# Performance work log

Measured on AMD Instinct MI355X. Metric: run time of the kernel, lower is better.

## Reference

```python
import jax, jax.numpy as jnp
import numpy as np

NUM_CLASSES = 10


def setup_inputs() -> dict:
    key = jax.random.key(0)
    k1, k2, k3 = jax.random.split(key, 3)
    N, M, D = 1024, 50000, 512
    x = jax.random.normal(k1, (N, D), dtype=jnp.float32)
    exemplars = jax.random.normal(k2, (M, D), dtype=jnp.float32)
    labels = jax.random.randint(k3, (M,), 0, NUM_CLASSES)
    Sigma_inv = jnp.ones((D,), dtype=jnp.float32)
    beta = jnp.ones((1,), dtype=jnp.float32)
    gamma = jnp.ones((1,), dtype=jnp.float32)
    return {"x": x, "exemplars": exemplars, "labels": labels,
            "Sigma_inv": Sigma_inv, "beta": beta, "gamma": gamma}


def reference(x, exemplars, labels, Sigma_inv, beta, gamma):
    # Weighted squared Mahalanobis distance via expanded quadratic form:
    # dist[n,m] = sum_d Sigma_inv[d] * (x[n,d] - e[m,d])^2
    #           = (x^2 @ S) + (e^2 @ S) - 2 * (x*S) @ e^T
    x_sq = jnp.einsum('nd,d->n', x * x, Sigma_inv)            # [N]
    e_sq = jnp.einsum('md,d->m', exemplars * exemplars, Sigma_inv)  # [M]
    cross = jnp.einsum('nd,md->nm', x * Sigma_inv, exemplars)  # [N, M]
    distances = x_sq[:, None] + e_sq[None, :] - 2.0 * cross    # [N, M]
    attention = jnp.exp(-beta[0] * distances)                  # [N, M]
    # Per-class masked sum == segment sum over exemplar labels.
    logits = jax.ops.segment_sum(attention.T, labels,
                                 num_segments=NUM_CLASSES).T   # [N, 10]
    return jax.nn.softmax(gamma[0] * logits, axis=1)
```

## Files before the change

### kernel.cpp

```cpp
#include <hip/hip_runtime.h>
#include <hip/hip_bf16.h>
#include <stdint.h>
#include <stddef.h>

#define N_TOT 1024
#define M_TOT 50000
#define M_PAD 50048
#define D_TOT 512
#define NC    10

typedef __attribute__((ext_vector_type(8))) __bf16 bf16x8;
typedef __attribute__((ext_vector_type(4))) float f32x4;
typedef __attribute__((ext_vector_type(4))) unsigned int u32x4;

union Frag16 { u32x4 q; bf16x8 b; unsigned short u[8]; };
union Pack8  { u32x4 q; unsigned short u[8]; };

__device__ __forceinline__ unsigned short f2bf(float x) {
  unsigned int u = __float_as_uint(x);
  unsigned int r = (u + 0x7fffu + ((u >> 16) & 1u)) >> 16;
  return (unsigned short)r;
}

__device__ __forceinline__ void gld_lds16(const void* g, void* l) {
  auto gp = (__attribute__((address_space(1))) unsigned int*)(uintptr_t)g;
  auto lp = (__attribute__((address_space(3))) unsigned int*)(uintptr_t)l;
  __builtin_amdgcn_global_load_lds(gp, lp, 16, 0, 0);
}

__global__ void prep_rows(const float* __restrict__ e, const float* __restrict__ x,
                          const float* __restrict__ S,
                          unsigned short* __restrict__ eb, unsigned short* __restrict__ xb,
                          float* __restrict__ e_sq, float* __restrict__ x_sq) {
  const int lane = threadIdx.x & 63;
  const int wid  = threadIdx.x >> 6;
  const int row  = blockIdx.x * 4 + wid;
  const int d0   = lane * 8;

  float4 s0 = *(const float4*)(S + d0);
  float4 s1 = *(const float4*)(S + d0 + 4);
  float ss[8] = {s0.x, s0.y, s0.z, s0.w, s1.x, s1.y, s1.z, s1.w};

  float acc = 0.f;
  Pack8 o;

  if (row < M_PAD) {
    if (row < M_TOT) {
      const float* src = e + (size_t)row * D_TOT + d0;
      float4 v0 = *(const float4*)src;
      float4 v1 = *(const float4*)(src + 4);
      float vv[8] = {v0.x, v0.y, v0.z, v0.w, v1.x, v1.y, v1.z, v1.w};
      #pragma unroll
      for (int j = 0; j < 8; ++j) { acc += ss[j] * vv[j] * vv[j]; o.u[j] = f2bf(vv[j]); }
    } else {
      #pragma unroll
      for (int j = 0; j < 8; ++j) o.u[j] = 0;
      acc = 0.f;
    }
    *(u32x4*)(eb + (size_t)row * D_TOT + d0) = o.q;
    #pragma unroll
    for (int off = 32; off; off >>= 1) acc += __shfl_down(acc, off);
    if (lane == 0) e_sq[row] = (row < M_TOT) ? acc : 1e30f;
  } else {
    const int xr = row - M_PAD;
    const float* src = x + (size_t)xr * D_TOT + d0;
    float4 v0 = *(const float4*)src;
    float4 v1 = *(const float4*)(src + 4);
    float vv[8] = {v0.x, v0.y, v0.z, v0.w, v1.x, v1.y, v1.z, v1.w};
    #pragma unroll
    for (int j = 0; j < 8; ++j) {
      float w = ss[j] * vv[j];
      acc += w * vv[j];
      o.u[j] = f2bf(w);
    }
    *(u32x4*)(xb + (size_t)xr * D_TOT + d0) = o.q;
    #pragma unroll
    for (int off = 32; off; off >>= 1) acc += __shfl_down(acc, off);
    if (lane == 0) x_sq[xr] = acc;
  }
}

__global__ void zero_f32(float* __restrict__ p, int n) {
  int i = blockIdx.x * 256 + threadIdx.x;
  if (i < n) p[i] = 0.f;
}

__launch_bounds__(256)
__global__ void gemm_fused(const unsigned short* __restrict__ xb,
                           const unsigned short* __restrict__ eb,
                           const float* __restrict__ x_sq, const float* __restrict__ e_sq,
                           const int* __restrict__ labels,
                           const float* __restrict__ betap,
                           float* __restrict__ logits) {
  __shared__ unsigned short As[2][128 * 32];
  __shared__ unsigned short Bs[2][128 * 32];
  __shared__ float cls[128 * NC];

  const int tid  = threadIdx.x;
  const int lane = tid & 63;
  const int wid  = tid >> 6;
  const int wr   = wid >> 1, wc = wid & 1;
  const int nt   = blockIdx.x;
  const int mt   = blockIdx.y;

  const int cA0 = wid * 128 + lane;
  const int cA1 = cA0 + 64;
  const unsigned short* gA0 = xb + (size_t)(nt * 128 + (cA0 >> 2)) * D_TOT + (cA0 & 3) * 8;
  const unsigned short* gA1 = xb + (size_t)(nt * 128 + (cA1 >> 2)) * D_TOT + (cA1 & 3) * 8;
  const unsigned short* gB0 = eb + (size_t)(mt * 128 + (cA0 >> 2)) * D_TOT + (cA0 & 3) * 8;
  const unsigned short* gB1 = eb + (size_t)(mt * 128 + (cA1 >> 2)) * D_TOT + (cA1 & 3) * 8;

  const f32x4 vzero = {0.f, 0.f, 0.f, 0.f};
  f32x4 acc[4][4];
  #pragma unroll
  for (int i = 0; i < 4; ++i)
    #pragma unroll
    for (int j = 0; j < 4; ++j) acc[i][j] = vzero;

  const int arow = wr * 64 + (lane & 15);
  const int brow = wc * 64 + (lane & 15);
  const int koff = (lane >> 4) * 8;

  #define STAGE(BUF, K0)                                    \
    do {                                                    \
      gld_lds16(gA0 + (K0), &As[(BUF)][cA0 * 8]);           \
      gld_lds16(gA1 + (K0), &As[(BUF)][cA1 * 8]);           \
      gld_lds16(gB0 + (K0), &Bs[(BUF)][cA0 * 8]);           \
      gld_lds16(gB1 + (K0), &Bs[(BUF)][cA1 * 8]);           \
    } while (0)

  #define COMPUTE(BUF)                                                            \
    do {                                                                          \
      Frag16 fa[4], fb[4];                                                        \
      _Pragma("unroll")                                                           \
      for (int i = 0; i < 4; ++i)                                                 \
        fa[i].q = *(const u32x4*)(&As[(BUF)][(arow + i * 16) * 32 + koff]);       \
      _Pragma("unroll")                                                           \
      for (int j = 0; j < 4; ++j)                                                 \
        fb[j].q = *(const u32x4*)(&Bs[(BUF)][(brow + j * 16) * 32 + koff]);       \
      _Pragma("unroll")                                                           \
      for (int i = 0; i < 4; ++i)                                                 \
        _Pragma("unroll")                                                         \
        for (int j = 0; j < 4; ++j)                                               \
          acc[i][j] = __builtin_amdgcn_mfma_f32_16x16x32_bf16(fa[i].b, fb[j].b,   \
                                                              acc[i][j], 0, 0, 0);\
    } while (0)

  STAGE(0, 0);
  #pragma unroll 2
  for (int ks = 0; ks < 15; ++ks) {
    const int cur = ks & 1;
    STAGE(cur ^ 1, (ks + 1) * 32);
    asm volatile("s_waitcnt vmcnt(4)" ::: "memory");
    __builtin_amdgcn_s_barrier();
    asm volatile("" ::: "memory");
    COMPUTE(cur);
    asm volatile("s_waitcnt lgkmcnt(0)" ::: "memory");
    __builtin_amdgcn_sched_barrier(0);
    __builtin_amdgcn_s_barrier();
  }
  asm volatile("s_waitcnt vmcnt(0)" ::: "memory");
  __builtin_amdgcn_s_barrier();
  asm volatile("" ::: "memory");
  COMPUTE(1);
  #undef STAGE
  #undef COMPUTE

  __syncthreads();
  for (int t = tid; t < 128 * NC; t += 256) cls[t] = 0.f;
  __syncthreads();

  const float beta = betap[0];
  const int mbase = mt * 128 + wc * 64 + (lane & 15);
  int   lab[4]; float esq[4]; bool mv[4];
  #pragma unroll
  for (int j = 0; j < 4; ++j) {
    const int m = mbase + j * 16;
    mv[j]  = (m < M_TOT);
    esq[j] = e_sq[m];
    lab[j] = mv[j] ? labels[m] : 0;
  }

  #pragma unroll
  for (int i = 0; i < 4; ++i) {
    #pragma unroll
    for (int r = 0; r < 4; ++r) {
      const int nloc = wr * 64 + i * 16 + (lane >> 4) * 4 + r;
      const float xs = x_sq[nt * 128 + nloc];
      #pragma unroll
      for (int j = 0; j < 4; ++j) {
        if (!mv[j]) continue;
        const float dist = xs + esq[j] - 2.0f * acc[i][j][r];
        const float a = __expf(-beta * dist);
        if (a != 0.0f) atomicAdd(&cls[nloc * NC + lab[j]], a);
      }
    }
  }
  __syncthreads();
  for (int t = tid; t < 128 * NC; t += 256) {
    const float v = cls[t];
    if (v != 0.0f) atomicAdd(&logits[(size_t)(nt * 128 + (t / NC)) * NC + (t % NC)], v);
  }
}

__global__ void softmax_out(const float* __restrict__ logits,
                            const float* __restrict__ gammap,
                            float* __restrict__ out) {
  const int n = blockIdx.x * blockDim.x + threadIdx.x;
  if (n >= N_TOT) return;
  const float g = gammap[0];
  float v[NC], mx = -3.4e38f;
  #pragma unroll
  for (int c = 0; c < NC; ++c) { v[c] = g * logits[n * NC + c]; mx = fmaxf(mx, v[c]); }
  float s = 0.f;
  #pragma unroll
  for (int c = 0; c < NC; ++c) { v[c] = __expf(v[c] - mx); s += v[c]; }
  const float inv = 1.0f / s;
  #pragma unroll
  for (int c = 0; c < NC; ++c) out[n * NC + c] = v[c] * inv;
}

extern "C" void kernel_launch(void* const* d_in, const int* in_sizes, int n_in,
                              void* d_out, int out_size, void* d_ws, size_t ws_size,
                              hipStream_t stream) {
  const float* x      = (const float*)d_in[0];
  const float* e      = (const float*)d_in[1];
  const int*   labels = (const int*)d_in[2];
  const float* S      = (const float*)d_in[3];
  const float* beta   = (const float*)d_in[4];
  const float* gamma  = (const float*)d_in[5];

  char* ws = (char*)d_ws;
  unsigned short* eb     = (unsigned short*)(ws);
  unsigned short* xb     = (unsigned short*)(ws + 51249152);
  float*          e_sq   = (float*)(ws + 52297728);
  float*          x_sq   = (float*)(ws + 52497920);
  float*          logits = (float*)(ws + 52502016);

  hipLaunchKernelGGL(prep_rows, dim3((M_PAD + N_TOT) / 4), dim3(256), 0, stream,
                     e, x, S, eb, xb, e_sq, x_sq);
  hipLaunchKernelGGL(zero_f32, dim3(40), dim3(256), 0, stream, logits, N_TOT * NC);
  hipLaunchKernelGGL(gemm_fused, dim3(8, 391), dim3(256), 0, stream,
                     xb, eb, x_sq, e_sq, labels, beta, logits);
  hipLaunchKernelGGL(softmax_out, dim3(4), dim3(256), 0, stream,
                     logits, gamma, (float*)d_out);
}
```

Measured before the change: 247.9 us.

## Triple-buffer GEMM k-loop, remap blocks for XCD locality, fold logits zeroing

Moves the GEMM's LDS staging from double to triple buffering, so two k-slices are in flight while the third is computed, and fully unrolls the k-loop. The grid becomes 1D with a block-index remap that gives each of 8 groups a contiguous range of exemplar tiles and all 8 x tiles per exemplar tile, aiming at L2 reuse across XCDs. This pads M to 392 tiles. The zero_f32 launch is folded into prep_rows to save one kernel launch. The extra buffer raises LDS use, which may reduce occupancy.

```diff
diff --git a/kernel.cpp b/kernel.cpp
--- a/kernel.cpp
+++ b/kernel.cpp
@@ -5,7 +5,8 @@
 
 #define N_TOT 1024
 #define M_TOT 50000
-#define M_PAD 50048
+#define M_PAD 50176
+#define MT_TILES 392
 #define D_TOT 512
 #define NC    10
 
@@ -31,7 +32,13 @@
 __global__ void prep_rows(const float* __restrict__ e, const float* __restrict__ x,
                           const float* __restrict__ S,
                           unsigned short* __restrict__ eb, unsigned short* __restrict__ xb,
-                          float* __restrict__ e_sq, float* __restrict__ x_sq) {
+                          float* __restrict__ e_sq, float* __restrict__ x_sq,
+                          float* __restrict__ logits) {
+  if (blockIdx.x < (N_TOT * NC + 255) / 256) {
+    const int i = blockIdx.x * 256 + threadIdx.x;
+    if (i < N_TOT * NC) logits[i] = 0.f;
+  }
+
   const int lane = threadIdx.x & 63;
   const int wid  = threadIdx.x >> 6;
   const int row  = blockIdx.x * 4 + wid;
@@ -80,11 +87,6 @@
   }
 }
 
-__global__ void zero_f32(float* __restrict__ p, int n) {
-  int i = blockIdx.x * 256 + threadIdx.x;
-  if (i < n) p[i] = 0.f;
-}
-
 __launch_bounds__(256)
 __global__ void gemm_fused(const unsigned short* __restrict__ xb,
                            const unsigned short* __restrict__ eb,
@@ -92,16 +94,20 @@
                            const int* __restrict__ labels,
                            const float* __restrict__ betap,
                            float* __restrict__ logits) {
-  __shared__ unsigned short As[2][128 * 32];
-  __shared__ unsigned short Bs[2][128 * 32];
+  __shared__ unsigned short As[3][128 * 32];
+  __shared__ unsigned short Bs[3][128 * 32];
   __shared__ float cls[128 * NC];
 
   const int tid  = threadIdx.x;
   const int lane = tid & 63;
   const int wid  = tid >> 6;
   const int wr   = wid >> 1, wc = wid & 1;
-  const int nt   = blockIdx.x;
-  const int mt   = blockIdx.y;
+
+  const int bid = blockIdx.x;
+  const int c   = bid & 7;
+  const int k_  = bid >> 3;
+  const int mt  = c * 49 + (k_ >> 3);
+  const int nt  = k_ & 7;
 
   const int cA0 = wid * 128 + lane;
   const int cA1 = cA0 + 64;
@@ -147,22 +153,28 @@
     } while (0)
 
   STAGE(0, 0);
-  #pragma unroll 2
-  for (int ks = 0; ks < 15; ++ks) {
-    const int cur = ks & 1;
-    STAGE(cur ^ 1, (ks + 1) * 32);
-    asm volatile("s_waitcnt vmcnt(4)" ::: "memory");
+  STAGE(1, 32);
+  #pragma unroll
+  for (int ks = 0; ks < 14; ++ks) {
+    const int nb = (ks + 2) % 3;
+    const int cb = ks % 3;
+    STAGE(nb, (ks + 2) * 32);
+    asm volatile("s_waitcnt vmcnt(8)" ::: "memory");
     __builtin_amdgcn_s_barrier();
     asm volatile("" ::: "memory");
-    COMPUTE(cur);
+    COMPUTE(cb);
     asm volatile("s_waitcnt lgkmcnt(0)" ::: "memory");
     __builtin_amdgcn_sched_barrier(0);
     __builtin_amdgcn_s_barrier();
   }
+  asm volatile("s_waitcnt vmcnt(4)" ::: "memory");
+  __builtin_amdgcn_s_barrier();
+  asm volatile("" ::: "memory");
+  COMPUTE(2);
   asm volatile("s_waitcnt vmcnt(0)" ::: "memory");
   __builtin_amdgcn_s_barrier();
   asm volatile("" ::: "memory");
-  COMPUTE(1);
+  COMPUTE(0);
   #undef STAGE
   #undef COMPUTE
 
@@ -232,15 +244,14 @@
 
   char* ws = (char*)d_ws;
   unsigned short* eb     = (unsigned short*)(ws);
-  unsigned short* xb     = (unsigned short*)(ws + 51249152);
-  float*          e_sq   = (float*)(ws + 52297728);
-  float*          x_sq   = (float*)(ws + 52497920);
-  float*          logits = (float*)(ws + 52502016);
+  unsigned short* xb     = (unsigned short*)(ws + 51380224);
+  float*          e_sq   = (float*)(ws + 52428800);
+  float*          x_sq   = (float*)(ws + 52629504);
+  float*          logits = (float*)(ws + 52633600);
 
   hipLaunchKernelGGL(prep_rows, dim3((M_PAD + N_TOT) / 4), dim3(256), 0, stream,
-                     e, x, S, eb, xb, e_sq, x_sq);
-  hipLaunchKernelGGL(zero_f32, dim3(40), dim3(256), 0, stream, logits, N_TOT * NC);
-  hipLaunchKernelGGL(gemm_fused, dim3(8, 391), dim3(256), 0, stream,
+                     e, x, S, eb, xb, e_sq, x_sq, logits);
+  hipLaunchKernelGGL(gemm_fused, dim3(8 * MT_TILES), dim3(256), 0, stream,
                      xb, eb, x_sq, e_sq, labels, beta, logits);
   hipLaunchKernelGGL(softmax_out, dim3(4), dim3(256), 0, stream,
                      logits, gamma, (float*)d_out);
```

After: 252.5 us. Within noise of the previous version (+1.8%).
